# Kernel optimization log

Hardware: AMD Instinct MI355X
Metric: run time of the kernel (lower is better)

The kernel has to match this reference:

```python
import jax, jax.numpy as jnp
import numpy as np
import math

D_MODEL = 1024
D_STATE = 128
D_CONV = 4
EXPAND = 2
HEADDIM = 64
NGROUPS = 1
D_INNER = EXPAND * D_MODEL            # 2048
D_SSM = D_INNER                       # d_ssm defaults to d_inner
NHEADS = D_SSM // HEADDIM             # 32
CONV_DIM = D_SSM + 2 * NGROUPS * D_STATE   # 2304
D_IN_PROJ = 2 * D_INNER + 2 * NGROUPS * D_STATE + NHEADS  # 4384
EPS = 1e-5
DT_MIN, DT_MAX = 1e-3, 1e-1


def setup_inputs() -> dict:
    key = jax.random.key(0)
    ks = jax.random.split(key, 8)
    u = jax.random.normal(ks[0], (2, 4096, D_MODEL), dtype=jnp.float32)
    W_in = jax.random.normal(ks[1], (D_IN_PROJ, D_MODEL), dtype=jnp.float32) * 0.02
    conv_w = jax.random.normal(ks[2], (CONV_DIM, D_CONV), dtype=jnp.float32) * 0.1
    conv_b = jnp.zeros((CONV_DIM,), dtype=jnp.float32)
    # dt_bias init as in the module: inv-softplus of dt ~ logU(dt_min, dt_max)
    dt = jnp.exp(jax.random.uniform(ks[3], (NHEADS,)) * (math.log(DT_MAX) - math.log(DT_MIN)) + math.log(DT_MIN))
    dt_bias = dt + jnp.log(-jnp.expm1(-dt))
    A_log = jnp.log(jax.random.uniform(ks[4], (NHEADS,), minval=1.0, maxval=16.0))
    D = jnp.ones((NHEADS,), dtype=jnp.float32)
    norm_w = jnp.ones((D_SSM,), dtype=jnp.float32)
    W_out = jax.random.normal(ks[5], (D_MODEL, D_INNER), dtype=jnp.float32) * 0.02
    return {"u": u, "W_in": W_in, "conv_w": conv_w, "conv_b": conv_b,
            "dt_bias": dt_bias, "A_log": A_log, "D": D, "norm_w": norm_w, "W_out": W_out}


def _mamba2_forward(u, W_in, conv_w, conv_b, dt_bias, A_log, D, norm_w, W_out):
    b, L, _ = u.shape
    zxbcdt = jnp.einsum('bld,ed->ble', u, W_in)  # (b, L, D_IN_PROJ)
    z = zxbcdt[..., :D_SSM]
    xBC = zxbcdt[..., D_SSM:D_SSM + CONV_DIM]
    dt = zxbcdt[..., D_SSM + CONV_DIM:]                     # (b, L, H)
    dt = jax.nn.softplus(dt + dt_bias)                      # (b, L, H)

    # causal depthwise conv1d + SiLU (channel-last, kernel width D_CONV)
    xp = jnp.pad(xBC, ((0, 0), (D_CONV - 1, 0), (0, 0)))
    conv = conv_b
    for w in range(D_CONV):
        conv = conv + xp[:, w:w + L, :] * conv_w[:, w]
    xBC = jax.nn.silu(conv)

    x = xBC[..., :D_SSM].reshape(b, L, NHEADS, HEADDIM)     # (b, L, H, P)
    B = xBC[..., D_SSM:D_SSM + D_STATE]                     # (b, L, N), ngroups=1
    C = xBC[..., D_SSM + D_STATE:]                          # (b, L, N)

    A = -jnp.exp(A_log)                                     # (H,)
    dA = jnp.exp(dt * A)                                    # (b, L, H)
    dtx = dt[..., None] * x                                 # (b, L, H, P)

    # selective state-space scan over time: h_t = h_{t-1}*dA_t + dt_t*x_t (x) B_t
    def step(h, inp):
        dA_t, dtx_t, B_t, C_t = inp                        # (b,H), (b,H,P), (b,N), (b,N)
        h = h * dA_t[:, :, None, None] + jnp.einsum('bhp,bn->bhpn', dtx_t, B_t)
        y_t = jnp.einsum('bhpn,bn->bhp', h, C_t)
        return h, y_t

    h0 = jnp.zeros((b, NHEADS, HEADDIM, D_STATE), dtype=u.dtype)
    inputs = (jnp.moveaxis(dA, 1, 0), jnp.moveaxis(dtx, 1, 0),
              jnp.moveaxis(B, 1, 0), jnp.moveaxis(C, 1, 0))
    _, y = jax.lax.scan(step, h0, inputs)                   # (L, b, H, P)
    y = jnp.moveaxis(y, 0, 1) + x * D[None, None, :, None]  # D skip per head
    y = y.reshape(b, L, D_SSM)

    # gated RMSNorm (norm_before_gate=False): normalize(y * silu(z)) * weight
    g = y * jax.nn.silu(z)
    g = g * jax.lax.rsqrt(jnp.mean(g * g, axis=-1, keepdims=True) + EPS) * norm_w
    return jnp.einsum('ble,de->bld', g, W_out)              # (b, L, D_MODEL)


def reference(u, W_in, conv_w, conv_b, dt_bias, A_log, D, norm_w, W_out):
    return _mamba2_forward(u, W_in, conv_w, conv_b, dt_bias, A_log, D, norm_w, W_out)
```

## Files before the change

kernel.cpp:

```cpp
#include <hip/hip_runtime.h>
#include <hip/hip_bf16.h>
#include <cstdint>

#define BB     2
#define LSEQ   4096
#define DM     1024
#define DSSM   2048
#define NH     32
#define HD     64
#define DS     128
#define NPROJ  4384
#define NPAD   4480
#define CONVD  2304
#define ROWS   (BB*LSEQ)
#define CHUNK  128
#define NCH    (LSEQ/CHUNK)
#define NBHC   (BB*NH*NCH)

typedef __bf16 bf16x8 __attribute__((ext_vector_type(8)));
typedef __bf16 bf16x4v __attribute__((ext_vector_type(4)));
typedef float  f32x4  __attribute__((ext_vector_type(4)));
typedef float  f32x16 __attribute__((ext_vector_type(16)));

__device__ __forceinline__ __bf16 to_bf(float f) {
    __hip_bfloat16 h = __float2bfloat16(f);
    return *(__bf16*)&h;
}

__device__ __forceinline__ void direct_load16(const void* gp, void* lp) {
    typedef const __attribute__((address_space(1))) unsigned int* gptr_t;
    typedef __attribute__((address_space(3))) unsigned int* lptr_t;
    __builtin_amdgcn_global_load_lds((gptr_t)(uintptr_t)gp,
                                     (lptr_t)(unsigned int)(uintptr_t)lp,
                                     16, 0, 0);
}

#define N1 ((size_t)ROWS * DM)
#define N2 ((size_t)NPAD * DM)
#define N3 ((size_t)DM * DSSM)
#define NREAL ((size_t)NPROJ * DM)

__global__ __launch_bounds__(256) void convert_all(const float* __restrict__ u,
                                                   const float* __restrict__ W_in,
                                                   const float* __restrict__ W_out,
                                                   __hip_bfloat16* __restrict__ ub,
                                                   __hip_bfloat16* __restrict__ winb,
                                                   __hip_bfloat16* __restrict__ woutb) {
    size_t i4 = ((size_t)blockIdx.x * 256 + threadIdx.x) * 4;
    const float* src;
    __hip_bfloat16* dst;
    size_t j;
    if (i4 < N1) { src = u; dst = ub; j = i4; }
    else if (i4 < N1 + N2) {
        j = i4 - N1;
        if (j >= NREAL) {
            ushort4 z = {0, 0, 0, 0};
            *(ushort4*)&winb[j] = z;
            return;
        }
        src = W_in; dst = winb;
    } else { src = W_out; dst = woutb; j = i4 - N1 - N2; }
    float4 v = *(const float4*)&src[j];
    __hip_bfloat16 o[4] = {__float2bfloat16(v.x), __float2bfloat16(v.y),
                           __float2bfloat16(v.z), __float2bfloat16(v.w)};
    *(ushort4*)&dst[j] = *(ushort4*)o;
}

__device__ __forceinline__ void storeC(float v, float* p) { *p = v; }
__device__ __forceinline__ void storeC(float v, __hip_bfloat16* p) { *p = __float2bfloat16(v); }

template <typename CT>
__global__ __launch_bounds__(256) void gemm_bt(const __hip_bfloat16* __restrict__ A,
                                               const __hip_bfloat16* __restrict__ B,
                                               CT* __restrict__ C,
                                               int M, int N, int K, int lda, int ldc) {
    __shared__ __bf16 lA[2][128 * 32];
    __shared__ __bf16 lB[2][128 * 32];
    const int tid = threadIdx.x;
    const int wv = tid >> 6, ln = tid & 63;

    const int gridM = M >> 7, gridN = N >> 7;
    const int pid = blockIdx.x;
    const int gsize = 8 * gridN;
    const int g = pid / gsize;
    const int first_m = g * 8;
    const int sz = min(8, gridM - first_m);
    const int m0 = (first_m + (pid % gsize) % sz) * 128;
    const int n0 = ((pid % gsize) / sz) * 128;

    const int wrow = (wv >> 1) * 64, wcol = (wv & 1) * 64;
    const int l31 = ln & 31, khalf = ln >> 5;
    const int sw = (l31 >> 2) & 3;

    f32x16 acc[2][2] = {};

    const int scol = (((ln & 3) ^ ((ln >> 4) & 3))) * 8;
    const int sr0 = wv * 16 + (ln >> 2);
    const int sr1 = (4 + wv) * 16 + (ln >> 2);

    const __hip_bfloat16* Ab = A + (size_t)m0 * lda;
    const __hip_bfloat16* Bb = B + (size_t)n0 * K;

    auto issue = [&](int buf, int k0) {
        direct_load16(Ab + (size_t)sr0 * lda + k0 + scol, &lA[buf][wv * 512]);
        direct_load16(Ab + (size_t)sr1 * lda + k0 + scol, &lA[buf][(4 + wv) * 512]);
        direct_load16(Bb + (size_t)sr0 * K + k0 + scol, &lB[buf][wv * 512]);
        direct_load16(Bb + (size_t)sr1 * K + k0 + scol, &lB[buf][(4 + wv) * 512]);
    };
    auto compute = [&](int buf) {
        #pragma unroll
        for (int ks = 0; ks < 2; ++ks) {
            const int ce = ((ks * 2 + khalf) ^ sw) * 8;
            bf16x8 af[2], bfr[2];
            #pragma unroll
            for (int tm = 0; tm < 2; ++tm)
                af[tm]  = *(const bf16x8*)&lA[buf][(wrow + tm * 32 + l31) * 32 + ce];
            #pragma unroll
            for (int tn = 0; tn < 2; ++tn)
                bfr[tn] = *(const bf16x8*)&lB[buf][(wcol + tn * 32 + l31) * 32 + ce];
            #pragma unroll
            for (int tm = 0; tm < 2; ++tm)
                #pragma unroll
                for (int tn = 0; tn < 2; ++tn)
                    acc[tm][tn] = __builtin_amdgcn_mfma_f32_32x32x16_bf16(af[tm], bfr[tn], acc[tm][tn], 0, 0, 0);
        }
    };

    issue(0, 0);
    const int nb = K / 32;
    for (int it = 0; it < nb; it += 2) {
        __syncthreads();
        if (it + 1 < nb) issue(1, (it + 1) * 32);
        compute(0);
        __syncthreads();
        if (it + 2 < nb) issue(0, (it + 2) * 32);
        compute(1);
    }

    #pragma unroll
    for (int tm = 0; tm < 2; ++tm) {
        #pragma unroll
        for (int tn = 0; tn < 2; ++tn) {
            const int rbase = m0 + wrow + tm * 32 + 4 * khalf;
            const int c0 = n0 + wcol + tn * 32 + l31;
            #pragma unroll
            for (int r = 0; r < 16; ++r) {
                const int row = rbase + (r & 3) + 8 * (r >> 2);
                storeC(acc[tm][tn][r], &C[(size_t)row * ldc + c0]);
            }
        }
    }
}

__global__ __launch_bounds__(256) void conv_fused(const __hip_bfloat16* __restrict__ zx,
                                                  const float* __restrict__ conv_w,
                                                  const float* __restrict__ conv_b,
                                                  const float* __restrict__ dt_bias,
                                                  __hip_bfloat16* __restrict__ xT,
                                                  __hip_bfloat16* __restrict__ Bv,
                                                  __hip_bfloat16* __restrict__ Cv,
                                                  __hip_bfloat16* __restrict__ BT,
                                                  float* __restrict__ dtv) {
    const int ct = blockIdx.x;
    const int rb = blockIdx.y * 64;
    const int tid = threadIdx.x;
    const int b = rb >> 12, l0 = rb & (LSEQ - 1);

    if (ct == 36) {
        const int r = tid >> 2, h8 = (tid & 3) * 8;
        const int gr = rb + r;
        bf16x8 v8 = *(const bf16x8*)&zx[(size_t)gr * NPAD + DSSM + CONVD + h8];
        float o[8];
        #pragma unroll
        for (int j = 0; j < 8; ++j) {
            float v = (float)v8[j] + dt_bias[h8 + j];
            o[j] = (v > 20.f) ? v : log1pf(__expf(v));
        }
        *(float4*)&dtv[(size_t)gr * NH + h8]     = *(float4*)&o[0];
        *(float4*)&dtv[(size_t)gr * NH + h8 + 4] = *(float4*)&o[4];
        return;
    }

    __shared__ __bf16 t[64][72];
    const int c0 = ct * 64;
    const int sc = (tid & 7) * 8;
    const int r2 = (tid >> 3) * 2;
    const int gc = c0 + sc;

    float cb[8];
    *(float4*)&cb[0] = *(const float4*)&conv_b[gc];
    *(float4*)&cb[4] = *(const float4*)&conv_b[gc + 4];
    float4 cw[8];
    #pragma unroll
    for (int j = 0; j < 8; ++j) cw[j] = *(const float4*)&conv_w[(gc + j) * 4];

    float in[5][8];
    #pragma unroll
    for (int i = 0; i < 5; ++i) {
        int ll = l0 + r2 - 3 + i;
        if (ll >= 0) {
            bf16x8 v = *(const bf16x8*)&zx[(size_t)(b * LSEQ + ll) * NPAD + DSSM + gc];
            #pragma unroll
            for (int j = 0; j < 8; ++j) in[i][j] = (float)v[j];
        } else {
            #pragma unroll
            for (int j = 0; j < 8; ++j) in[i][j] = 0.f;
        }
    }

    bf16x8 o0, o1;
    #pragma unroll
    for (int j = 0; j < 8; ++j) {
        float a0 = cb[j] + cw[j].x * in[0][j] + cw[j].y * in[1][j] + cw[j].z * in[2][j] + cw[j].w * in[3][j];
        float a1 = cb[j] + cw[j].x * in[1][j] + cw[j].y * in[2][j] + cw[j].z * in[3][j] + cw[j].w * in[4][j];
        o0[j] = to_bf(a0 / (1.f + __expf(-a0)));
        o1[j] = to_bf(a1 / (1.f + __expf(-a1)));
    }

    if (ct >= 32 && ct < 34) {
        const int bc = gc - 2048;
        *(bf16x8*)&Bv[(size_t)(rb + r2) * DS + bc]     = o0;
        *(bf16x8*)&Bv[(size_t)(rb + r2 + 1) * DS + bc] = o1;
    } else if (ct >= 34) {
        const int cc = gc - 2176;
        *(bf16x8*)&Cv[(size_t)(rb + r2) * DS + cc]     = o0;
        *(bf16x8*)&Cv[(size_t)(rb + r2 + 1) * DS + cc] = o1;
    }

    if (ct < 34) {
        #pragma unroll
        for (int j = 0; j < 8; ++j) { t[sc + j][r2] = o0[j]; t[sc + j][r2 + 1] = o1[j]; }
        __syncthreads();
        const int trow = tid >> 3, tcolg = (tid & 7) * 8;
        #pragma unroll
        for (int hfl = 0; hfl < 2; ++hfl) {
            const int rr = hfl * 32 + trow;
            bf16x8 o;
            #pragma unroll
            for (int j = 0; j < 8; ++j) o[j] = t[rr][tcolg + j];
            __hip_bfloat16* dst = (ct < 32)
                ? &xT[(size_t)(b * DSSM + c0 + rr) * LSEQ + l0 + tcolg]
                : &BT[(size_t)(b * DS + (c0 - 2048) + rr) * LSEQ + l0 + tcolg];
            *(bf16x8*)dst = o;
        }
    }
}

__global__ __launch_bounds__(256) void chunk_local(const __hip_bfloat16* __restrict__ xT,
                                                   const __hip_bfloat16* __restrict__ BT,
                                                   const float* __restrict__ dtv,
                                                   const float* __restrict__ A_log,
                                                   __hip_bfloat16* __restrict__ sst,
                                                   float* __restrict__ lcg) {
    __shared__ __bf16 lXT[4][HD * 32];
    __shared__ __bf16 lBT[4][DS * 32];
    __shared__ float sc[2][CHUNK];
    __shared__ float lw[CHUNK];

    const int bid = blockIdx.x;
    const int c = bid & 31, hh = (bid >> 5) & 31, b = bid >> 10;
    const int tid = threadIdx.x;
    const int wv = tid >> 6, ln = tid & 63;
    const int r0 = b * LSEQ + c * CHUNK;
    const int s0 = c * CHUNK;

    {
        const int row16 = ln >> 2, col8 = (ln & 3) * 8;
        const __hip_bfloat16* Bb = BT + (size_t)b * DS * LSEQ + s0 + wv * 32 + col8;
        #pragma unroll
        for (int j = 0; j < 8; ++j)
            direct_load16(Bb + (size_t)(j * 16 + row16) * LSEQ, &lBT[wv][j * 512]);
    }

    float dt_s = 0.f;
    if (tid < CHUNK) {
        dt_s = dtv[(size_t)(r0 + tid) * NH + hh];
        sc[0][tid] = -__expf(A_log[hh]) * dt_s;
    }
    __syncthreads();
    int src = 0;
    for (int off = 1; off < CHUNK; off <<= 1) {
        if (tid < CHUNK)
            sc[src ^ 1][tid] = sc[src][tid] + ((tid >= off) ? sc[src][tid - off] : 0.f);
        __syncthreads();
        src ^= 1;
    }
    if (tid < CHUNK) {
        float Lc = sc[src][tid];
        lcg[(size_t)bid * CHUNK + tid] = Lc;
        lw[tid] = dt_s * __expf(sc[src][CHUNK - 1] - Lc);
    }
    __syncthreads();

    {
        const int p = tid >> 2, ks = tid & 3;
        const __hip_bfloat16* xr = xT + (size_t)(b * DSSM + hh * HD + p) * LSEQ + s0 + ks * 32;
        #pragma unroll
        for (int v = 0; v < 4; ++v) {
            bf16x8 xv = *(const bf16x8*)&xr[v * 8];
            float4 w0 = *(const float4*)&lw[ks * 32 + v * 8];
            float4 w1 = *(const float4*)&lw[ks * 32 + v * 8 + 4];
            bf16x8 o;
            o[0] = to_bf((float)xv[0] * w0.x); o[1] = to_bf((float)xv[1] * w0.y);
            o[2] = to_bf((float)xv[2] * w0.z); o[3] = to_bf((float)xv[3] * w0.w);
            o[4] = to_bf((float)xv[4] * w1.x); o[5] = to_bf((float)xv[5] * w1.y);
            o[6] = to_bf((float)xv[6] * w1.z); o[7] = to_bf((float)xv[7] * w1.w);
            *(bf16x8*)&lXT[ks][p * 32 + v * 8] = o;
        }
    }
    __syncthreads();

    const int lane15 = ln & 15, quad = ln >> 4;
    f32x4 acc[4][2] = {};
    #pragma unroll
    for (int ks = 0; ks < 4; ++ks) {
        bf16x8 af[4], bf[2];
        #pragma unroll
        for (int mi = 0; mi < 4; ++mi)
            af[mi] = *(const bf16x8*)&lXT[ks][(mi * 16 + lane15) * 32 + quad * 8];
        #pragma unroll
        for (int ni = 0; ni < 2; ++ni)
            bf[ni] = *(const bf16x8*)&lBT[ks][(wv * 32 + ni * 16 + lane15) * 32 + quad * 8];
        #pragma unroll
        for (int mi = 0; mi < 4; ++mi)
            #pragma unroll
            for (int ni = 0; ni < 2; ++ni)
                acc[mi][ni] = __builtin_amdgcn_mfma_f32_16x16x32_bf16(af[mi], bf[ni], acc[mi][ni], 0, 0, 0);
    }

    __hip_bfloat16* sb = sst + (size_t)bid * (HD * DS);
    #pragma unroll
    for (int mi = 0; mi < 4; ++mi)
        #pragma unroll
        for (int ni = 0; ni < 2; ++ni) {
            int p0 = mi * 16 + quad * 4;
            int n0 = wv * 32 + ni * 16 + lane15;
            #pragma unroll
            for (int r = 0; r < 4; ++r)
                sb[(size_t)(p0 + r) * DS + n0] = __float2bfloat16(acc[mi][ni][r]);
        }
}

__global__ __launch_bounds__(256) void chunk_scan(__hip_bfloat16* __restrict__ sst,
                                                  const float* __restrict__ lcg) {
    const int bid = blockIdx.x;
    const int bh = bid >> 5;
    const int elem = (bid & 31) * 256 + threadIdx.x;
    float h = 0.f;
    size_t base = (size_t)bh * NCH * (HD * DS) + elem;
    const float* lg = lcg + (size_t)bh * NCH * CHUNK;
    for (int cc = 0; cc < NCH; ++cc) {
        float cq = __expf(lg[cc * CHUNK + CHUNK - 1]);
        size_t a = base + (size_t)cc * (HD * DS);
        float sv = __bfloat162float(sst[a]);
        sst[a] = __float2bfloat16(h);
        h = cq * h + sv;
    }
}

__global__ __launch_bounds__(256) void chunk_y(const __hip_bfloat16* __restrict__ xT,
                                               const __hip_bfloat16* __restrict__ Bv,
                                               const __hip_bfloat16* __restrict__ Cv,
                                               const float* __restrict__ dtv,
                                               const float* __restrict__ lcg,
                                               const __hip_bfloat16* __restrict__ sst,
                                               const float* __restrict__ Dv,
                                               __hip_bfloat16* __restrict__ y) {
    __shared__ __bf16 lC[4][128 * 32];
    __shared__ __bf16 lB[4][128 * 32];
    __shared__ float sLc[CHUNK];
    __shared__ float sdt[CHUNK];

    const int bid = blockIdx.x;
    const int c = bid & 31, hh = (bid >> 5) & 31, b = bid >> 10;
    const int tid = threadIdx.x;
    const int wv = tid >> 6, ln = tid & 63;
    const int lane15 = ln & 15, quad = ln >> 4;
    const int r0 = b * LSEQ + c * CHUNK;

    const __hip_bfloat16* Cb = Cv + (size_t)r0 * DS;
    const __hip_bfloat16* Bb = Bv + (size_t)r0 * DS;
    const __hip_bfloat16* Hb = sst + (size_t)bid * (HD * DS);

    {
        const int i3 = ln & 3, i4 = ln >> 2;
        #pragma unroll
        for (int j = 0; j < 8; ++j) {
            direct_load16(Cb + (size_t)(j * 16 + i4) * DS + wv * 32 + i3 * 8, &lC[wv][j * 512]);
            direct_load16(Bb + (size_t)(j * 16 + i4) * DS + wv * 32 + i3 * 8, &lB[wv][j * 512]);
        }
    }
    if (tid < CHUNK) {
        sLc[tid] = lcg[(size_t)bid * CHUNK + tid];
        sdt[tid] = dtv[(size_t)(r0 + tid) * NH + hh];
    }
    __syncthreads();

    const int wrow = (wv >> 1) * 64, wcol = (wv & 1) * 64;
    const int wr2 = wv * 32;
    f32x4 acc[4][4] = {};
    f32x4 accY[2][4] = {};

    #pragma unroll
    for (int ks = 0; ks < 4; ++ks) {
        bf16x8 af[4], bfr[4], af2[2], bh[4];
        #pragma unroll
        for (int i = 0; i < 4; ++i) {
            af[i]  = *(const bf16x8*)&lB[ks][(wrow + i * 16 + lane15) * 32 + quad * 8];
            bfr[i] = *(const bf16x8*)&lC[ks][(wcol + i * 16 + lane15) * 32 + quad * 8];
        }
        #pragma unroll
        for (int mi = 0; mi < 2; ++mi)
            af2[mi] = *(const bf16x8*)&lC[ks][(wr2 + mi * 16 + lane15) * 32 + quad * 8];
        #pragma unroll
        for (int ni = 0; ni < 4; ++ni)
            bh[ni] = *(const bf16x8*)&Hb[(size_t)(ni * 16 + lane15) * DS + ks * 32 + quad * 8];
        #pragma unroll
        for (int mi = 0; mi < 4; ++mi)
            #pragma unroll
            for (int ni = 0; ni < 4; ++ni)
                acc[mi][ni] = __builtin_amdgcn_mfma_f32_16x16x32_bf16(af[mi], bfr[ni], acc[mi][ni], 0, 0, 0);
        #pragma unroll
        for (int mi = 0; mi < 2; ++mi)
            #pragma unroll
            for (int ni = 0; ni < 4; ++ni)
                accY[mi][ni] = __builtin_amdgcn_mfma_f32_16x16x32_bf16(af2[mi], bh[ni], accY[mi][ni], 0, 0, 0);
    }

    #pragma unroll
    for (int mi = 0; mi < 2; ++mi)
        #pragma unroll
        for (int r = 0; r < 4; ++r) {
            float cum = __expf(sLc[wr2 + mi * 16 + quad * 4 + r]);
            #pragma unroll
            for (int ni = 0; ni < 4; ++ni) accY[mi][ni][r] *= cum;
        }

    __syncthreads();

    {
        const int row16 = ln >> 2, col8 = (ln & 3) * 8;
        const __hip_bfloat16* xr = xT + (size_t)(b * DSSM + hh * HD) * LSEQ + c * CHUNK + wv * 32 + col8;
        #pragma unroll
        for (int j = 0; j < 4; ++j)
            direct_load16(xr + (size_t)(j * 16 + row16) * LSEQ, &lB[wv][j * 512]);
    }

    #pragma unroll
    for (int mi = 0; mi < 4; ++mi) {
        const int sb = wrow + mi * 16 + quad * 4;
        float el[4], dt4[4];
        #pragma unroll
        for (int r = 0; r < 4; ++r) { el[r] = sLc[sb + r]; dt4[r] = sdt[sb + r]; }
        #pragma unroll
        for (int ni = 0; ni < 4; ++ni) {
            const int t = wcol + ni * 16 + lane15;
            const float Lct = sLc[t];
            bf16x4v o;
            #pragma unroll
            for (int r = 0; r < 4; ++r) {
                const int s = sb + r;
                float v = (s <= t) ? acc[mi][ni][r] * __expf(Lct - el[r]) * dt4[r] : 0.f;
                o[r] = to_bf(v);
            }
            *(bf16x4v*)&lC[sb >> 5][t * 32 + (sb & 31)] = o;
        }
    }
    __syncthreads();

    #pragma unroll
    for (int ks = 0; ks < 4; ++ks) {
        bf16x8 af2[2], bx[4];
        #pragma unroll
        for (int mi = 0; mi < 2; ++mi)
            af2[mi] = *(const bf16x8*)&lC[ks][(wr2 + mi * 16 + lane15) * 32 + quad * 8];
        #pragma unroll
        for (int ni = 0; ni < 4; ++ni)
            bx[ni] = *(const bf16x8*)&lB[ks][(ni * 16 + lane15) * 32 + quad * 8];
        #pragma unroll
        for (int mi = 0; mi < 2; ++mi)
            #pragma unroll
            for (int ni = 0; ni < 4; ++ni)
                accY[mi][ni] = __builtin_amdgcn_mfma_f32_16x16x32_bf16(af2[mi], bx[ni], accY[mi][ni], 0, 0, 0);
    }

    const float dsc = Dv[hh];
    #pragma unroll
    for (int mi = 0; mi < 2; ++mi)
        #pragma unroll
        for (int ni = 0; ni < 4; ++ni) {
            const int p0 = ni * 16 + lane15;
            #pragma unroll
            for (int r = 0; r < 4; ++r) {
                const int t = wr2 + mi * 16 + quad * 4 + r;
                accY[mi][ni][r] += dsc * (float)lB[t >> 5][p0 * 32 + (t & 31)];
            }
        }

    __hip_bfloat16* yb = y + (size_t)r0 * DSSM + hh * HD;
    #pragma unroll
    for (int mi = 0; mi < 2; ++mi)
        #pragma unroll
        for (int ni = 0; ni < 4; ++ni) {
            const int p0 = ni * 16 + lane15;
            #pragma unroll
            for (int r = 0; r < 4; ++r) {
                const int t = wr2 + mi * 16 + quad * 4 + r;
                yb[(size_t)t * DSSM + p0] = __float2bfloat16(accY[mi][ni][r]);
            }
        }
}

__global__ __launch_bounds__(256) void gnorm_kernel(const __hip_bfloat16* __restrict__ y,
                                                    __hip_bfloat16* __restrict__ zx,
                                                    const float* __restrict__ nw) {
    const int r = blockIdx.x;
    const int tid = threadIdx.x;
    const int c = tid * 8;
    const size_t off = (size_t)r * DSSM + c;
    bf16x8 yv8 = *(const bf16x8*)&y[off];
    bf16x8 zv8 = *(const bf16x8*)&zx[(size_t)r * NPAD + c];
    float gv[8];
    float ss = 0.f;
    #pragma unroll
    for (int i = 0; i < 8; ++i) {
        float yv = (float)yv8[i];
        float z = (float)zv8[i];
        float gq = yv * (z / (1.f + __expf(-z)));
        gv[i] = gq;
        ss += gq * gq;
    }
    #pragma unroll
    for (int o = 32; o; o >>= 1) ss += __shfl_xor(ss, o, 64);
    __shared__ float ws4[4];
    if ((tid & 63) == 0) ws4[tid >> 6] = ss;
    __syncthreads();
    const float tot = ws4[0] + ws4[1] + ws4[2] + ws4[3];
    const float scale = rsqrtf(tot * (1.f / (float)DSSM) + 1e-5f);
    bf16x8 o;
    #pragma unroll
    for (int i = 0; i < 8; ++i) o[i] = to_bf(gv[i] * scale * nw[c + i]);
    *(bf16x8*)&zx[(size_t)r * NPAD + DSSM + c] = o;
}

extern "C" void kernel_launch(void* const* d_in, const int* in_sizes, int n_in,
                              void* d_out, int out_size, void* d_ws, size_t ws_size,
                              hipStream_t stream) {
    const float* u       = (const float*)d_in[0];
    const float* W_in    = (const float*)d_in[1];
    const float* conv_w  = (const float*)d_in[2];
    const float* conv_b  = (const float*)d_in[3];
    const float* dt_bias = (const float*)d_in[4];
    const float* A_log   = (const float*)d_in[5];
    const float* Dv      = (const float*)d_in[6];
    const float* norm_w  = (const float*)d_in[7];
    const float* W_out   = (const float*)d_in[8];
    float* out = (float*)d_out;

    char* ws = (char*)d_ws;
    size_t off = 0;
    auto alloc = [&](size_t bytes) { char* p = ws + off; off += (bytes + 255) & ~(size_t)255; return p; };

    __hip_bfloat16* ub    = (__hip_bfloat16*)alloc((size_t)ROWS * DM * 2);
    __hip_bfloat16* winb  = (__hip_bfloat16*)alloc((size_t)NPAD * DM * 2);
    __hip_bfloat16* woutb = (__hip_bfloat16*)alloc((size_t)DM * DSSM * 2);
    __hip_bfloat16* zx    = (__hip_bfloat16*)alloc((size_t)ROWS * NPAD * 2);
    __hip_bfloat16* yb    = (__hip_bfloat16*)alloc((size_t)ROWS * DSSM * 2);
    __hip_bfloat16* sst   = (__hip_bfloat16*)alloc((size_t)NBHC * HD * DS * 2);
    __hip_bfloat16* xT    = (__hip_bfloat16*)alloc((size_t)ROWS * DSSM * 2);
    __hip_bfloat16* BT    = (__hip_bfloat16*)alloc((size_t)ROWS * DS * 2);

    __hip_bfloat16* Bvp = (__hip_bfloat16*)ub;
    __hip_bfloat16* Cvp = Bvp + (size_t)ROWS * DS;
    float*          dtv = (float*)(Cvp + (size_t)ROWS * DS);
    float*          lcg = (float*)winb;

    convert_all<<<(unsigned)((N1 + N2 + N3) / 4 / 256), 256, 0, stream>>>(
        u, W_in, W_out, ub, winb, woutb);

    gemm_bt<__hip_bfloat16><<<(ROWS / 128) * (NPAD / 128), 256, 0, stream>>>(
        ub, winb, zx, ROWS, NPAD, DM, DM, NPAD);

    conv_fused<<<dim3(37, ROWS / 64), 256, 0, stream>>>(
        zx, conv_w, conv_b, dt_bias, xT, Bvp, Cvp, BT, dtv);

    chunk_local<<<NBHC, 256, 0, stream>>>(xT, BT, dtv, A_log, sst, lcg);
    chunk_scan<<<NBHC, 256, 0, stream>>>(sst, lcg);
    chunk_y<<<NBHC, 256, 0, stream>>>(xT, Bvp, Cvp, dtv, lcg, sst, Dv, yb);

    gnorm_kernel<<<ROWS, 256, 0, stream>>>(yb, zx, norm_w);

    gemm_bt<float><<<(ROWS / 128) * (DM / 128), 256, 0, stream>>>(
        zx + DSSM, woutb, out, ROWS, DM, DSSM, NPAD, DM);
}
```

Before: 377.4 us.

## Single-buffer GEMM LDS for higher occupancy; batch loads in chunk scan

The bf16 GEMM drops its double-buffered LDS pipeline in favour of a single buffer with load-sync-compute-sync per K step, and adds a launch-bounds minimum of 4 blocks per CU. Halving shared memory is meant to let more blocks run at once and hide latency through occupancy instead of software prefetch. The cost is that loads no longer overlap compute within a block, and there are extra barriers. Separately, the inter-chunk state scan now loads all 32 chunk states into registers up front, runs the recurrence, then writes them back, so the memory loads are no longer serialized behind the dependent recurrence.

```diff
diff --git a/kernel.cpp b/kernel.cpp
--- a/kernel.cpp
+++ b/kernel.cpp
@@ -70,12 +70,12 @@
 __device__ __forceinline__ void storeC(float v, __hip_bfloat16* p) { *p = __float2bfloat16(v); }
 
 template <typename CT>
-__global__ __launch_bounds__(256) void gemm_bt(const __hip_bfloat16* __restrict__ A,
-                                               const __hip_bfloat16* __restrict__ B,
-                                               CT* __restrict__ C,
-                                               int M, int N, int K, int lda, int ldc) {
-    __shared__ __bf16 lA[2][128 * 32];
-    __shared__ __bf16 lB[2][128 * 32];
+__global__ __launch_bounds__(256, 4) void gemm_bt(const __hip_bfloat16* __restrict__ A,
+                                                  const __hip_bfloat16* __restrict__ B,
+                                                  CT* __restrict__ C,
+                                                  int M, int N, int K, int lda, int ldc) {
+    __shared__ __bf16 lA[128 * 32];
+    __shared__ __bf16 lB[128 * 32];
     const int tid = threadIdx.x;
     const int wv = tid >> 6, ln = tid & 63;
 
@@ -101,40 +101,30 @@
     const __hip_bfloat16* Ab = A + (size_t)m0 * lda;
     const __hip_bfloat16* Bb = B + (size_t)n0 * K;
 
-    auto issue = [&](int buf, int k0) {
-        direct_load16(Ab + (size_t)sr0 * lda + k0 + scol, &lA[buf][wv * 512]);
-        direct_load16(Ab + (size_t)sr1 * lda + k0 + scol, &lA[buf][(4 + wv) * 512]);
-        direct_load16(Bb + (size_t)sr0 * K + k0 + scol, &lB[buf][wv * 512]);
-        direct_load16(Bb + (size_t)sr1 * K + k0 + scol, &lB[buf][(4 + wv) * 512]);
-    };
-    auto compute = [&](int buf) {
+    for (int k0 = 0; k0 < K; k0 += 32) {
+        direct_load16(Ab + (size_t)sr0 * lda + k0 + scol, &lA[wv * 512]);
+        direct_load16(Ab + (size_t)sr1 * lda + k0 + scol, &lA[(4 + wv) * 512]);
+        direct_load16(Bb + (size_t)sr0 * K + k0 + scol, &lB[wv * 512]);
+        direct_load16(Bb + (size_t)sr1 * K + k0 + scol, &lB[(4 + wv) * 512]);
+        __syncthreads();
+
         #pragma unroll
         for (int ks = 0; ks < 2; ++ks) {
             const int ce = ((ks * 2 + khalf) ^ sw) * 8;
             bf16x8 af[2], bfr[2];
             #pragma unroll
             for (int tm = 0; tm < 2; ++tm)
-                af[tm]  = *(const bf16x8*)&lA[buf][(wrow + tm * 32 + l31) * 32 + ce];
+                af[tm]  = *(const bf16x8*)&lA[(wrow + tm * 32 + l31) * 32 + ce];
             #pragma unroll
             for (int tn = 0; tn < 2; ++tn)
-                bfr[tn] = *(const bf16x8*)&lB[buf][(wcol + tn * 32 + l31) * 32 + ce];
+                bfr[tn] = *(const bf16x8*)&lB[(wcol + tn * 32 + l31) * 32 + ce];
             #pragma unroll
             for (int tm = 0; tm < 2; ++tm)
                 #pragma unroll
                 for (int tn = 0; tn < 2; ++tn)
                     acc[tm][tn] = __builtin_amdgcn_mfma_f32_32x32x16_bf16(af[tm], bfr[tn], acc[tm][tn], 0, 0, 0);
         }
-    };
-
-    issue(0, 0);
-    const int nb = K / 32;
-    for (int it = 0; it < nb; it += 2) {
         __syncthreads();
-        if (it + 1 < nb) issue(1, (it + 1) * 32);
-        compute(0);
-        __syncthreads();
-        if (it + 2 < nb) issue(0, (it + 2) * 32);
-        compute(1);
     }
 
     #pragma unroll
@@ -346,16 +336,26 @@
     const int bid = blockIdx.x;
     const int bh = bid >> 5;
     const int elem = (bid & 31) * 256 + threadIdx.x;
-    float h = 0.f;
     size_t base = (size_t)bh * NCH * (HD * DS) + elem;
     const float* lg = lcg + (size_t)bh * NCH * CHUNK;
+
+    float v[NCH];
+    #pragma unroll
+    for (int cc = 0; cc < NCH; ++cc)
+        v[cc] = __bfloat162float(sst[base + (size_t)cc * (HD * DS)]);
+
+    float h = 0.f;
+    #pragma unroll
     for (int cc = 0; cc < NCH; ++cc) {
         float cq = __expf(lg[cc * CHUNK + CHUNK - 1]);
-        size_t a = base + (size_t)cc * (HD * DS);
-        float sv = __bfloat162float(sst[a]);
-        sst[a] = __float2bfloat16(h);
+        float sv = v[cc];
+        v[cc] = h;
         h = cq * h + sv;
     }
+
+    #pragma unroll
+    for (int cc = 0; cc < NCH; ++cc)
+        sst[base + (size_t)cc * (HD * DS)] = __float2bfloat16(v[cc]);
 }
 
 __global__ __launch_bounds__(256) void chunk_y(const __hip_bfloat16* __restrict__ xT,
```

Measured after the change: 384.7 us. No clear change (+1.9%).
